# Kernel tuning notes

Measured on AMD Instinct MI355X. Metric: run time of the kernel, lower is better.

Reference implementation:

```python
import jax, jax.numpy as jnp
import numpy as np


def _to_complex(t):
    # last dim 2 = (real, imag) -> complex64
    return jax.lax.complex(t[..., 0], t[..., 1])


def setup_inputs() -> dict:
    key = jax.random.key(0)
    k1, k2, k3, k4 = jax.random.split(key, 4)
    N, C_out, C_in, H, Wf = 2, 64, 3, 256, 129  # Wf = 256//2 + 1 (rfft width)
    X = jax.random.normal(k1, (N, 1, C_in, H, Wf, 2), dtype=jnp.float32)
    D = jax.random.normal(k2, (N, C_out, C_in, H, Wf, 2), dtype=jnp.float32)
    Y = jax.random.normal(k3, (N, C_out, 1, H, Wf, 2), dtype=jnp.float32)
    # alpha is a positive penalty weight; offset away from 0 to avoid blow-up in Z/alpha
    alpha = jax.random.uniform(k4, (N, 1, 1, 1), dtype=jnp.float32) + 0.5
    x_size = np.array([256, 256], dtype=np.int64)  # spatial size for irfft2
    return {"X": X, "D": D, "Y": Y, "alpha": alpha, "x_size": x_size}


def reference(X, D, Y, alpha, x_size):
    C_in = X.shape[2]
    Xc = _to_complex(X)  # (N,1,C_in,H,Wf)
    Dc = _to_complex(D)  # (N,C_out,C_in,H,Wf)
    Yc = _to_complex(Y)  # (N,C_out,1,H,Wf)
    # alpha.unsqueeze(-1).unsqueeze(-1)/C_in: in complex repr one extra axis suffices
    a = (alpha / C_in)[..., None]  # (N,1,1,1,1), real, broadcasts over (N,C_out,C_in,H,Wf)
    Dconj = jnp.conj(Dc)
    Z = Yc * Dc + a * Xc  # (N,C_out,C_in,H,Wf)
    factor1 = Z / a
    numerator = jnp.sum(Dconj * Z, axis=2, keepdims=True)  # (N,C_out,1,H,Wf)
    # csum adds a real scalar (alpha^2) to the real part only
    denominator = a * jnp.sum(Dconj * Dc, axis=2, keepdims=True) + a ** 2
    factor2 = Dc * (numerator / denominator)  # (N,C_out,C_in,H,Wf)
    Xhat = jnp.mean(factor1 - factor2, axis=1)  # (N,C_in,H,Wf)
    Hs, Ws = int(x_size[0]), int(x_size[1])
    # torch.irfft(signal_ndim=2, normalized=False) == full (1/n-normalized) inverse rfft2
    return jnp.fft.irfftn(Xhat, s=(Hs, Ws), axes=(-2, -1))
```

## Files before the change

kernel.cpp:

```cpp
#include <hip/hip_runtime.h>
#include <math.h>

#define H_   256
#define Wf_  129
#define HWf_ 33024
#define NHW_ 66048
#define CIN_ 3
#define COUT_ 64

__global__ __launch_bounds__(256) void solve_stage1(
    const float2* __restrict__ X, const float2* __restrict__ D,
    const float2* __restrict__ Y, const float* __restrict__ alpha,
    float2* __restrict__ Xhat)
{
    const int tid = threadIdx.x;
    const int cog = tid >> 6;
    const int l   = tid & 63;
    const int p   = blockIdx.x * 64 + l;
    const int n   = p / HWf_;
    const int hw  = p - n * HWf_;

    const float a    = alpha[n] * (1.0f / 3.0f);
    const float inva = 1.0f / a;
    const float a2   = a * a;

    const float2 x0 = X[n * (CIN_ * HWf_) + 0 * HWf_ + hw];
    const float2 x1 = X[n * (CIN_ * HWf_) + 1 * HWf_ + hw];
    const float2 x2 = X[n * (CIN_ * HWf_) + 2 * HWf_ + hw];

    const float2* Dp = D + (size_t)n * (COUT_ * CIN_ * HWf_)
                         + (size_t)(cog * 16) * (CIN_ * HWf_) + hw;
    const float2* Yp = Y + (size_t)n * (COUT_ * HWf_)
                         + (size_t)(cog * 16) * HWf_ + hw;

    float ar0 = 0.f, ai0 = 0.f, ar1 = 0.f, ai1 = 0.f, ar2 = 0.f, ai2 = 0.f;

#pragma unroll 4
    for (int co = 0; co < 16; ++co) {
        float2 y  = Yp[co * HWf_];
        float2 d0 = Dp[co * (CIN_ * HWf_) + 0 * HWf_];
        float2 d1 = Dp[co * (CIN_ * HWf_) + 1 * HWf_];
        float2 d2 = Dp[co * (CIN_ * HWf_) + 2 * HWf_];

        float s2 = d0.x*d0.x + d0.y*d0.y + d1.x*d1.x + d1.y*d1.y
                 + d2.x*d2.x + d2.y*d2.y;
        float sr = d0.x*x0.x + d0.y*x0.y + d1.x*x1.x + d1.y*x1.y
                 + d2.x*x2.x + d2.y*x2.y;
        float si = d0.x*x0.y - d0.y*x0.x + d1.x*x1.y - d1.y*x1.x
                 + d2.x*x2.y - d2.y*x2.x;

        float nr = y.x * s2 + a * sr;
        float ni = y.y * s2 + a * si;
        float invden = 1.0f / (a * s2 + a2);
        float cr = nr * invden, cim = ni * invden;

        float tr = y.x * inva - cr;
        float ti = y.y * inva - cim;

        ar0 += d0.x*tr - d0.y*ti;  ai0 += d0.x*ti + d0.y*tr;
        ar1 += d1.x*tr - d1.y*ti;  ai1 += d1.x*ti + d1.y*tr;
        ar2 += d2.x*tr - d2.y*ti;  ai2 += d2.x*ti + d2.y*tr;
    }

    __shared__ float red[6][256];
    red[0][tid] = ar0; red[1][tid] = ai0; red[2][tid] = ar1;
    red[3][tid] = ai1; red[4][tid] = ar2; red[5][tid] = ai2;
    __syncthreads();

    if (tid < 64) {
        float s[6];
#pragma unroll
        for (int c2 = 0; c2 < 6; ++c2)
            s[c2] = red[c2][tid] + red[c2][tid + 64]
                  + red[c2][tid + 128] + red[c2][tid + 192];
        const float inv64 = 1.0f / 64.0f;
        float2* o = Xhat + n * (CIN_ * HWf_) + hw;
        o[0]         = make_float2(x0.x + s[0] * inv64, x0.y + s[1] * inv64);
        o[HWf_]      = make_float2(x1.x + s[2] * inv64, x1.y + s[3] * inv64);
        o[2 * HWf_]  = make_float2(x2.x + s[4] * inv64, x2.y + s[5] * inv64);
    }
}

__global__ __launch_bounds__(256) void solve_stage2(
    const float2* __restrict__ in, float2* __restrict__ out)
{
    __shared__ float2 col[256];
    __shared__ float2 tw[256];

    const int b    = blockIdx.x;
    const int n_ci = b / Wf_;
    const int w    = b - n_ci * Wf_;
    const int h    = threadIdx.x;

    const float2* src = in + (size_t)n_ci * HWf_ + w;
    col[h] = src[h * Wf_];

    float sv, cv;
    sincosf((float)h * (float)(2.0 * M_PI / 256.0), &sv, &cv);
    tw[h] = make_float2(cv, sv);
    __syncthreads();

    float ar = 0.f, ai = 0.f;
#pragma unroll 8
    for (int k = 0; k < 256; ++k) {
        float2 v = col[k];
        float2 t = tw[(k * h) & 255];
        ar += v.x * t.x - v.y * t.y;
        ai += v.x * t.y + v.y * t.x;
    }

    float2* dst = out + (size_t)n_ci * HWf_ + w;
    dst[h * Wf_] = make_float2(ar * (1.0f / 256.0f), ai * (1.0f / 256.0f));
}

__global__ __launch_bounds__(256) void solve_stage3(
    const float2* __restrict__ in, float* __restrict__ out)
{
    __shared__ float2 row[Wf_];
    __shared__ float2 tw[256];

    const int b = blockIdx.x;
    const int m = threadIdx.x;

    if (m < Wf_) row[m] = in[(size_t)b * Wf_ + m];
    float sv, cv;
    sincosf((float)m * (float)(2.0 * M_PI / 256.0), &sv, &cv);
    tw[m] = make_float2(cv, sv);
    __syncthreads();

    float acc = 0.5f * row[0].x;
    float nyq = 0.5f * row[128].x;
    acc += (m & 1) ? -nyq : nyq;

#pragma unroll 8
    for (int k = 1; k < 128; ++k) {
        float2 v = row[k];
        float2 t = tw[(k * m) & 255];
        acc += v.x * t.x - v.y * t.y;
    }

    out[(size_t)b * 256 + m] = acc * (2.0f / 256.0f);
}

extern "C" void kernel_launch(void* const* d_in, const int* in_sizes, int n_in,
                              void* d_out, int out_size, void* d_ws, size_t ws_size,
                              hipStream_t stream) {
    const float2* X     = (const float2*)d_in[0];
    const float2* D     = (const float2*)d_in[1];
    const float2* Y     = (const float2*)d_in[2];
    const float*  alpha = (const float*)d_in[3];

    float2* ws1 = (float2*)d_ws;
    float2* ws2 = ws1 + (size_t)CIN_ * 2 * HWf_;

    solve_stage1<<<NHW_ / 64, 256, 0, stream>>>(X, D, Y, alpha, ws1);
    solve_stage2<<<2 * CIN_ * Wf_, 256, 0, stream>>>(ws1, ws2);
    solve_stage3<<<2 * CIN_ * H_, 256, 0, stream>>>(ws2, (float*)d_out);
}
```

Baseline: 219.1 us.

## Vectorize stage-1 loads to float4 and use twiddle recurrences with even/odd split in DFTs

Stage 1 now has each thread handle two adjacent frequency positions through float4 loads, over 4 output channels instead of 16, which raises per-thread memory width and the number of blocks. The closing reduction is reorganised through a larger shared buffer and written out by 192 threads. Stages 2 and 3 drop the shared twiddle table and instead generate twiddles by a rotation recurrence, reseeded with sincosf every 32 steps. They also exploit the even/odd symmetry so each of 128 threads produces two outputs. The recurrence may accumulate rounding error, and the new stage-1 layout adds shared-memory reduction traffic.

Measured after the change: 216.6 us. Within noise of the previous version (-1.1%).

```diff
diff --git a/kernel.cpp b/kernel.cpp
--- a/kernel.cpp
+++ b/kernel.cpp
@@ -4,156 +4,204 @@
 #define H_   256
 #define Wf_  129
 #define HWf_ 33024
-#define NHW_ 66048
 #define CIN_ 3
 #define COUT_ 64
+#define TW_  0.0245436926f
 
 __global__ __launch_bounds__(256) void solve_stage1(
-    const float2* __restrict__ X, const float2* __restrict__ D,
-    const float2* __restrict__ Y, const float* __restrict__ alpha,
-    float2* __restrict__ Xhat)
+    const float* __restrict__ X, const float* __restrict__ D,
+    const float* __restrict__ Y, const float* __restrict__ alpha,
+    float* __restrict__ Xhat)
 {
-    const int tid = threadIdx.x;
-    const int cog = tid >> 6;
-    const int l   = tid & 63;
-    const int p   = blockIdx.x * 64 + l;
-    const int n   = p / HWf_;
-    const int hw  = p - n * HWf_;
+    const int tid  = threadIdx.x;
+    const int pl   = tid & 15;
+    const int cog  = tid >> 4;
+    const int pair = blockIdx.x * 16 + pl;
+    const int pos0 = pair * 2;
+    const int n    = pos0 / HWf_;
+    const int hw0  = pos0 - n * HWf_;
 
     const float a    = alpha[n] * (1.0f / 3.0f);
     const float inva = 1.0f / a;
     const float a2   = a * a;
 
-    const float2 x0 = X[n * (CIN_ * HWf_) + 0 * HWf_ + hw];
-    const float2 x1 = X[n * (CIN_ * HWf_) + 1 * HWf_ + hw];
-    const float2 x2 = X[n * (CIN_ * HWf_) + 2 * HWf_ + hw];
-
-    const float2* Dp = D + (size_t)n * (COUT_ * CIN_ * HWf_)
-                         + (size_t)(cog * 16) * (CIN_ * HWf_) + hw;
-    const float2* Yp = Y + (size_t)n * (COUT_ * HWf_)
-                         + (size_t)(cog * 16) * HWf_ + hw;
-
-    float ar0 = 0.f, ai0 = 0.f, ar1 = 0.f, ai1 = 0.f, ar2 = 0.f, ai2 = 0.f;
-
-#pragma unroll 4
-    for (int co = 0; co < 16; ++co) {
-        float2 y  = Yp[co * HWf_];
-        float2 d0 = Dp[co * (CIN_ * HWf_) + 0 * HWf_];
-        float2 d1 = Dp[co * (CIN_ * HWf_) + 1 * HWf_];
-        float2 d2 = Dp[co * (CIN_ * HWf_) + 2 * HWf_];
-
-        float s2 = d0.x*d0.x + d0.y*d0.y + d1.x*d1.x + d1.y*d1.y
-                 + d2.x*d2.x + d2.y*d2.y;
-        float sr = d0.x*x0.x + d0.y*x0.y + d1.x*x1.x + d1.y*x1.y
-                 + d2.x*x2.x + d2.y*x2.y;
-        float si = d0.x*x0.y - d0.y*x0.x + d1.x*x1.y - d1.y*x1.x
-                 + d2.x*x2.y - d2.y*x2.x;
-
-        float nr = y.x * s2 + a * sr;
-        float ni = y.y * s2 + a * si;
-        float invden = 1.0f / (a * s2 + a2);
-        float cr = nr * invden, cim = ni * invden;
-
-        float tr = y.x * inva - cr;
-        float ti = y.y * inva - cim;
-
-        ar0 += d0.x*tr - d0.y*ti;  ai0 += d0.x*ti + d0.y*tr;
-        ar1 += d1.x*tr - d1.y*ti;  ai1 += d1.x*ti + d1.y*tr;
-        ar2 += d2.x*tr - d2.y*ti;  ai2 += d2.x*ti + d2.y*tr;
-    }
-
-    __shared__ float red[6][256];
-    red[0][tid] = ar0; red[1][tid] = ai0; red[2][tid] = ar1;
-    red[3][tid] = ai1; red[4][tid] = ar2; red[5][tid] = ai2;
+    float4 x[3];
+#pragma unroll
+    for (int ci = 0; ci < 3; ++ci)
+        x[ci] = *(const float4*)(X + ((size_t)(n * 3 + ci) * HWf_ + hw0) * 2);
+
+    const int co0 = cog * 4;
+    const float* Dp = D + ((size_t)(n * 64 + co0) * 3) * (HWf_ * 2) + hw0 * 2;
+    const float* Yp = Y + ((size_t)(n * 64 + co0)) * (HWf_ * 2) + hw0 * 2;
+
+    float acc[12];
+#pragma unroll
+    for (int q = 0; q < 12; ++q) acc[q] = 0.f;
+
+#pragma unroll
+    for (int co = 0; co < 4; ++co) {
+        float4 y  = *(const float4*)(Yp + (size_t)co * (HWf_ * 2));
+        float4 d0 = *(const float4*)(Dp + (size_t)(co * 3 + 0) * (HWf_ * 2));
+        float4 d1 = *(const float4*)(Dp + (size_t)(co * 3 + 1) * (HWf_ * 2));
+        float4 d2 = *(const float4*)(Dp + (size_t)(co * 3 + 2) * (HWf_ * 2));
+
+        {
+            float s2 = d0.x*d0.x + d0.y*d0.y + d1.x*d1.x + d1.y*d1.y
+                     + d2.x*d2.x + d2.y*d2.y;
+            float sr = d0.x*x[0].x + d0.y*x[0].y + d1.x*x[1].x + d1.y*x[1].y
+                     + d2.x*x[2].x + d2.y*x[2].y;
+            float si = d0.x*x[0].y - d0.y*x[0].x + d1.x*x[1].y - d1.y*x[1].x
+                     + d2.x*x[2].y - d2.y*x[2].x;
+            float nr = y.x * s2 + a * sr, ni = y.y * s2 + a * si;
+            float invden = 1.0f / (a * s2 + a2);
+            float tr = y.x * inva - nr * invden;
+            float ti = y.y * inva - ni * invden;
+            acc[0] += d0.x*tr - d0.y*ti;  acc[1] += d0.x*ti + d0.y*tr;
+            acc[2] += d1.x*tr - d1.y*ti;  acc[3] += d1.x*ti + d1.y*tr;
+            acc[4] += d2.x*tr - d2.y*ti;  acc[5] += d2.x*ti + d2.y*tr;
+        }
+        {
+            float s2 = d0.z*d0.z + d0.w*d0.w + d1.z*d1.z + d1.w*d1.w
+                     + d2.z*d2.z + d2.w*d2.w;
+            float sr = d0.z*x[0].z + d0.w*x[0].w + d1.z*x[1].z + d1.w*x[1].w
+                     + d2.z*x[2].z + d2.w*x[2].w;
+            float si = d0.z*x[0].w - d0.w*x[0].z + d1.z*x[1].w - d1.w*x[1].z
+                     + d2.z*x[2].w - d2.w*x[2].z;
+            float nr = y.z * s2 + a * sr, ni = y.w * s2 + a * si;
+            float invden = 1.0f / (a * s2 + a2);
+            float tr = y.z * inva - nr * invden;
+            float ti = y.w * inva - ni * invden;
+            acc[6]  += d0.z*tr - d0.w*ti;  acc[7]  += d0.z*ti + d0.w*tr;
+            acc[8]  += d1.z*tr - d1.w*ti;  acc[9]  += d1.z*ti + d1.w*tr;
+            acc[10] += d2.z*tr - d2.w*ti;  acc[11] += d2.z*ti + d2.w*tr;
+        }
+    }
+
+    __shared__ float red[16 * 192];
+    {
+        const int base = cog * 192 + pl * 12;
+#pragma unroll
+        for (int q = 0; q < 12; ++q) red[base + q] = acc[q];
+    }
     __syncthreads();
 
-    if (tid < 64) {
-        float s[6];
-#pragma unroll
-        for (int c2 = 0; c2 < 6; ++c2)
-            s[c2] = red[c2][tid] + red[c2][tid + 64]
-                  + red[c2][tid + 128] + red[c2][tid + 192];
-        const float inv64 = 1.0f / 64.0f;
-        float2* o = Xhat + n * (CIN_ * HWf_) + hw;
-        o[0]         = make_float2(x0.x + s[0] * inv64, x0.y + s[1] * inv64);
-        o[HWf_]      = make_float2(x1.x + s[2] * inv64, x1.y + s[3] * inv64);
-        o[2 * HWf_]  = make_float2(x2.x + s[4] * inv64, x2.y + s[5] * inv64);
-    }
-}
-
-__global__ __launch_bounds__(256) void solve_stage2(
+    if (tid < 192) {
+        float s = 0.f;
+#pragma unroll
+        for (int c = 0; c < 16; ++c) s += red[c * 192 + tid];
+        const int P   = tid / 12;
+        const int r   = tid - P * 12;
+        const int pos = r / 6;
+        const int rr  = r - pos * 6;
+        const int ci  = rr >> 1;
+        const int cc  = rr & 1;
+        const int gp  = (blockIdx.x * 16 + P) * 2 + pos;
+        const int hw  = gp - n * HWf_;
+        const size_t o = ((size_t)(n * 3 + ci) * HWf_ + hw) * 2 + cc;
+        Xhat[o] = X[o] + s * (1.0f / 64.0f);
+    }
+}
+
+__global__ __launch_bounds__(128) void solve_stage2(
     const float2* __restrict__ in, float2* __restrict__ out)
 {
     __shared__ float2 col[256];
-    __shared__ float2 tw[256];
 
     const int b    = blockIdx.x;
     const int n_ci = b / Wf_;
     const int w    = b - n_ci * Wf_;
-    const int h    = threadIdx.x;
+    const int t    = threadIdx.x;
 
     const float2* src = in + (size_t)n_ci * HWf_ + w;
-    col[h] = src[h * Wf_];
-
-    float sv, cv;
-    sincosf((float)h * (float)(2.0 * M_PI / 256.0), &sv, &cv);
-    tw[h] = make_float2(cv, sv);
+    col[t]       = src[t * Wf_];
+    col[t + 128] = src[(t + 128) * Wf_];
     __syncthreads();
 
-    float ar = 0.f, ai = 0.f;
-#pragma unroll 8
-    for (int k = 0; k < 256; ++k) {
-        float2 v = col[k];
-        float2 t = tw[(k * h) & 255];
-        ar += v.x * t.x - v.y * t.y;
-        ai += v.x * t.y + v.y * t.x;
+    float wc, wsn;
+    sincosf((float)t * TW_, &wsn, &wc);
+
+    float ar = 0.f, ai = 0.f, br = 0.f, bi = 0.f;
+    for (int kb = 0; kb < 8; ++kb) {
+        const int k0 = kb * 32;
+        float tr, ti;
+        {
+            const int m = (t * k0) & 255;
+            float s, c; sincosf((float)m * TW_, &s, &c);
+            tr = c; ti = s;
+        }
+#pragma unroll
+        for (int j = 0; j < 32; ++j) {
+            const float2 v = col[k0 + j];
+            const float pr = v.x * tr - v.y * ti;
+            const float pi = v.x * ti + v.y * tr;
+            ar += pr; ai += pi;
+            if ((k0 + j) & 1) { br -= pr; bi -= pi; }
+            else             { br += pr; bi += pi; }
+            const float nt = tr * wc - ti * wsn;
+            ti = tr * wsn + ti * wc;
+            tr = nt;
+        }
     }
 
     float2* dst = out + (size_t)n_ci * HWf_ + w;
-    dst[h * Wf_] = make_float2(ar * (1.0f / 256.0f), ai * (1.0f / 256.0f));
-}
-
-__global__ __launch_bounds__(256) void solve_stage3(
+    dst[t * Wf_]         = make_float2(ar * (1.0f / 256.0f), ai * (1.0f / 256.0f));
+    dst[(t + 128) * Wf_] = make_float2(br * (1.0f / 256.0f), bi * (1.0f / 256.0f));
+}
+
+__global__ __launch_bounds__(128) void solve_stage3(
     const float2* __restrict__ in, float* __restrict__ out)
 {
     __shared__ float2 row[Wf_];
-    __shared__ float2 tw[256];
 
     const int b = blockIdx.x;
-    const int m = threadIdx.x;
-
-    if (m < Wf_) row[m] = in[(size_t)b * Wf_ + m];
-    float sv, cv;
-    sincosf((float)m * (float)(2.0 * M_PI / 256.0), &sv, &cv);
-    tw[m] = make_float2(cv, sv);
+    const int t = threadIdx.x;
+
+    row[t] = in[(size_t)b * Wf_ + t];
+    if (t == 0) row[128] = in[(size_t)b * Wf_ + 128];
     __syncthreads();
 
-    float acc = 0.5f * row[0].x;
-    float nyq = 0.5f * row[128].x;
-    acc += (m & 1) ? -nyq : nyq;
-
-#pragma unroll 8
-    for (int k = 1; k < 128; ++k) {
-        float2 v = row[k];
-        float2 t = tw[(k * m) & 255];
-        acc += v.x * t.x - v.y * t.y;
-    }
-
-    out[(size_t)b * 256 + m] = acc * (2.0f / 256.0f);
+    float wc, wsn;
+    sincosf((float)t * TW_, &wsn, &wc);
+
+    float sa = 0.f, sb = 0.f;
+    for (int kb = 0; kb < 4; ++kb) {
+        const int k0 = kb * 32;
+        float tr, ti;
+        {
+            const int m = (t * k0) & 255;
+            float s, c; sincosf((float)m * TW_, &s, &c);
+            tr = c; ti = s;
+        }
+#pragma unroll
+        for (int j = 0; j < 32; ++j) {
+            const float2 v = row[k0 + j];
+            const float pr = v.x * tr - v.y * ti;
+            sa += pr;
+            if ((k0 + j) & 1) sb -= pr; else sb += pr;
+            const float nt = tr * wc - ti * wsn;
+            ti = tr * wsn + ti * wc;
+            tr = nt;
+        }
+    }
+
+    const float sgn  = (t & 1) ? -1.0f : 1.0f;
+    const float base = -0.5f * row[0].x + sgn * 0.5f * row[128].x;
+    out[(size_t)b * 256 + t]       = (sa + base) * (1.0f / 128.0f);
+    out[(size_t)b * 256 + t + 128] = (sb + base) * (1.0f / 128.0f);
 }
 
 extern "C" void kernel_launch(void* const* d_in, const int* in_sizes, int n_in,
                               void* d_out, int out_size, void* d_ws, size_t ws_size,
                               hipStream_t stream) {
-    const float2* X     = (const float2*)d_in[0];
-    const float2* D     = (const float2*)d_in[1];
-    const float2* Y     = (const float2*)d_in[2];
-    const float*  alpha = (const float*)d_in[3];
-
-    float2* ws1 = (float2*)d_ws;
-    float2* ws2 = ws1 + (size_t)CIN_ * 2 * HWf_;
-
-    solve_stage1<<<NHW_ / 64, 256, 0, stream>>>(X, D, Y, alpha, ws1);
-    solve_stage2<<<2 * CIN_ * Wf_, 256, 0, stream>>>(ws1, ws2);
-    solve_stage3<<<2 * CIN_ * H_, 256, 0, stream>>>(ws2, (float*)d_out);
-}
+    const float* X     = (const float*)d_in[0];
+    const float* D     = (const float*)d_in[1];
+    const float* Y     = (const float*)d_in[2];
+    const float* alpha = (const float*)d_in[3];
+
+    float* ws1 = (float*)d_ws;
+    float2* ws2 = (float2*)(ws1 + (size_t)CIN_ * 2 * HWf_ * 2);
+
+    solve_stage1<<<2064, 256, 0, stream>>>(X, D, Y, alpha, ws1);
+    solve_stage2<<<2 * CIN_ * Wf_, 128, 0, stream>>>((const float2*)ws1, ws2);
+    solve_stage3<<<2 * CIN_ * H_, 128, 0, stream>>>(ws2, (float*)d_out);
+}
```
